# Kernel tuning notes

Hardware: AMD Instinct MI355X
Metric: run time of the kernel (lower is better)

The kernel has to match this reference:

```python
import jax, jax.numpy as jnp
import numpy as np

N_NODES = 50000
LEAKY_SLOPE = 0.2


def _degrees(idx, n):
    d = jax.ops.segment_sum(jnp.ones_like(idx, dtype=jnp.float32), idx, num_segments=n)
    return jnp.clip(d, 1.0)  # DGL clamps zero degrees to 1


def _gcn_layer(x, W, b, src, dst, out_inv_sqrt, in_inv_sqrt):
    # norm='both': h = D_in^{-1/2} A D_out^{-1/2} x, then x @ W + b
    h = x * out_inv_sqrt[:, None]
    agg = jax.ops.segment_sum(jnp.take(h, src, axis=0), dst, num_segments=N_NODES)
    agg = agg * in_inv_sqrt[:, None]
    return agg @ W + b


def setup_inputs() -> dict:
    key = jax.random.key(0)
    k1, k2, k3, k4, k5 = jax.random.split(key, 5)
    E = 800000
    init_emb = jax.random.normal(k1, (N_NODES, 300), dtype=jnp.float32)
    W1 = jax.random.normal(k2, (300, 400), dtype=jnp.float32) * (1.0 / np.sqrt(300.0))
    b1 = jnp.zeros((400,), dtype=jnp.float32)
    W2 = jax.random.normal(k3, (400, 512), dtype=jnp.float32) * (1.0 / np.sqrt(400.0))
    b2 = jnp.zeros((512,), dtype=jnp.float32)
    src = jax.random.randint(k4, (E,), 0, N_NODES, dtype=jnp.int32)
    dst = jax.random.randint(k5, (E,), 0, N_NODES, dtype=jnp.int32)
    return {"init_emb": init_emb, "W1": W1, "b1": b1, "W2": W2, "b2": b2,
            "src": src, "dst": dst}


def reference(init_emb, W1, b1, W2, b2, src, dst):
    out_inv_sqrt = jax.lax.rsqrt(_degrees(src, N_NODES))  # D_out^{-1/2}
    in_inv_sqrt = jax.lax.rsqrt(_degrees(dst, N_NODES))   # D_in^{-1/2}
    x = _gcn_layer(init_emb, W1, b1, src, dst, out_inv_sqrt, in_inv_sqrt)
    x = jnp.where(x >= 0, x, LEAKY_SLOPE * x)  # LeakyReLU(0.2); dropout = identity (eval)
    x = _gcn_layer(x, W2, b2, src, dst, out_inv_sqrt, in_inv_sqrt)
    return x
```

## Files before the change

### kernel.cpp

```cpp
#include <hip/hip_runtime.h>
#include <hip/hip_fp16.h>

#define NN   50000
#define NNP  50048
#define D0   300
#define K1   320
#define N1   400
#define K2   448
#define N2   512
#define NBLK 196

typedef __attribute__((ext_vector_type(8))) short bf16x8;
typedef __attribute__((ext_vector_type(4))) float f32x4;
typedef __attribute__((ext_vector_type(2))) float f32x2;
typedef __attribute__((ext_vector_type(4))) unsigned int u32x4;

__device__ __forceinline__ unsigned short f2bf(float x) {
    union { float f; unsigned u; } v; v.f = x;
    unsigned r = v.u + 0x7fffu + ((v.u >> 16) & 1u);
    return (unsigned short)(r >> 16);
}

__global__ __launch_bounds__(256) void pre_kernel(const int* __restrict__ src,
                                                  const int* __restrict__ dst,
                                                  int* __restrict__ cnt_s,
                                                  int* __restrict__ cnt_d, int E,
                                                  const float* __restrict__ W1,
                                                  const float* __restrict__ W2,
                                                  unsigned short* __restrict__ T1,
                                                  unsigned short* __restrict__ T2) {
    int tid = blockIdx.x * 256 + threadIdx.x;
    if (tid < E) {
        atomicAdd(&cnt_s[src[tid]], 1);
        atomicAdd(&cnt_d[dst[tid]], 1);
        return;
    }
    int u = tid - E;
    if (u < K2 * K1) {
        int n = u / K1, k = u - n * K1;
        float v = (n < N1 && k < D0) ? W1[k * N1 + n] : 0.f;
        T1[u] = f2bf(v);
    } else {
        u -= K2 * K1;
        if (u >= N2 * K2) return;
        int n = u / K2, k = u - n * K2;
        float v = (k < N1) ? W2[k * N2 + n] : 0.f;
        T2[u] = f2bf(v);
    }
}

__global__ __launch_bounds__(256) void scan_blk_kernel(const int* __restrict__ cnt,
                                                       int* __restrict__ offs,
                                                       int* __restrict__ bsum) {
    __shared__ int sh[256];
    int t = threadIdx.x, g = blockIdx.x * 256 + t;
    int v = (g < NN) ? cnt[g] : 0;
    sh[t] = v;
    __syncthreads();
    for (int off = 1; off < 256; off <<= 1) {
        int u = (t >= off) ? sh[t - off] : 0;
        __syncthreads();
        sh[t] += u;
        __syncthreads();
    }
    if (g < NN) offs[g] = sh[t] - v;
    if (t == 255) bsum[blockIdx.x] = sh[255];
}

__global__ __launch_bounds__(256) void scan_fix_kernel(int* __restrict__ offs,
                                                       const int* __restrict__ bsum,
                                                       const int* __restrict__ cnt_s,
                                                       const int* __restrict__ cnt_d,
                                                       float* __restrict__ deg_s,
                                                       float* __restrict__ deg_d, int E) {
    __shared__ int sh[256];
    int t = threadIdx.x;
    int v = (t < NBLK) ? bsum[t] : 0;
    sh[t] = v;
    __syncthreads();
    for (int off = 1; off < 256; off <<= 1) {
        int u = (t >= off) ? sh[t - off] : 0;
        __syncthreads();
        sh[t] += u;
        __syncthreads();
    }
    int myboff = (blockIdx.x > 0) ? sh[blockIdx.x - 1] : 0;
    int g = blockIdx.x * 256 + t;
    if (g < NN) {
        offs[g] += myboff;
        deg_s[g] = rsqrtf(fmaxf((float)cnt_s[g], 1.0f));
        deg_d[g] = rsqrtf(fmaxf((float)cnt_d[g], 1.0f));
    }
    if (g == NN) offs[NN] = E;
}

__global__ __launch_bounds__(256) void scat_emb_kernel(
    const int* __restrict__ src, const int* __restrict__ dst,
    const int* __restrict__ offs, int* __restrict__ cursor,
    int* __restrict__ ssrc, int E,
    const float* __restrict__ emb, const float* __restrict__ deg_s,
    __half* __restrict__ embh) {
    int tid = blockIdx.x * 256 + threadIdx.x;
    if (tid < E) {
        int d = dst[tid];
        int pos = atomicAdd(&cursor[d], 1);
        ssrc[offs[d] + pos] = src[tid];
        return;
    }
    int u = tid - E;
    const int CPR = K1 / 4;
    if (u >= NN * CPR) return;
    int node = u / CPR, c = u - node * CPR;
    int f = 4 * c;
    __half h[4] = {__half(0.f), __half(0.f), __half(0.f), __half(0.f)};
    if (f < D0) {
        float sc = deg_s[node];
        float4 v = *(const float4*)(emb + (size_t)node * D0 + f);
        h[0] = __float2half(v.x * sc); h[1] = __float2half(v.y * sc);
        h[2] = __float2half(v.z * sc); h[3] = __float2half(v.w * sc);
    }
    *(uint2*)(embh + (size_t)node * K1 + f) = *(uint2*)h;
}

template <int KP>
__global__ __launch_bounds__(256) void agg_h_kernel(
    const __half* __restrict__ X, const int* __restrict__ offs,
    const int* __restrict__ ssrc, const float* __restrict__ nscale,
    unsigned short* __restrict__ O) {
    constexpr int D8 = KP / 8;
    int node = blockIdx.x * 4 + (threadIdx.x >> 6);
    if (node >= NNP) return;
    int l = threadIdx.x & 63;
    bool act = l < D8;
    const uint4* Xq = (const uint4*)X;

    float a[8] = {0.f, 0.f, 0.f, 0.f, 0.f, 0.f, 0.f, 0.f};

#define ACCUM(U) { const __half2* hp = (const __half2*)&(U);                        \
                   float2 f0 = __half22float2(hp[0]), f1 = __half22float2(hp[1]);   \
                   float2 f2 = __half22float2(hp[2]), f3 = __half22float2(hp[3]);   \
                   a[0] += f0.x; a[1] += f0.y; a[2] += f1.x; a[3] += f1.y;          \
                   a[4] += f2.x; a[5] += f2.y; a[6] += f3.x; a[7] += f3.y; }

    if (node < NN) {
        int j = offs[node], end = offs[node + 1];
        for (; j + 8 <= end; j += 8) {
            uint4 u0, u1, u2, u3, u4, u5, u6, u7;
            int s0 = ssrc[j + 0], s1 = ssrc[j + 1], s2 = ssrc[j + 2], s3 = ssrc[j + 3];
            int s4 = ssrc[j + 4], s5 = ssrc[j + 5], s6 = ssrc[j + 6], s7 = ssrc[j + 7];
            if (act) {
                u0 = Xq[(size_t)s0 * D8 + l]; u1 = Xq[(size_t)s1 * D8 + l];
                u2 = Xq[(size_t)s2 * D8 + l]; u3 = Xq[(size_t)s3 * D8 + l];
                u4 = Xq[(size_t)s4 * D8 + l]; u5 = Xq[(size_t)s5 * D8 + l];
                u6 = Xq[(size_t)s6 * D8 + l]; u7 = Xq[(size_t)s7 * D8 + l];
                ACCUM(u0); ACCUM(u1); ACCUM(u2); ACCUM(u3);
                ACCUM(u4); ACCUM(u5); ACCUM(u6); ACCUM(u7);
            }
        }
        for (; j + 2 <= end; j += 2) {
            int s0 = ssrc[j + 0], s1 = ssrc[j + 1];
            if (act) {
                uint4 u0 = Xq[(size_t)s0 * D8 + l];
                uint4 u1 = Xq[(size_t)s1 * D8 + l];
                ACCUM(u0); ACCUM(u1);
            }
        }
        for (; j < end; ++j) {
            int s0 = ssrc[j];
            if (act) { uint4 u0 = Xq[(size_t)s0 * D8 + l]; ACCUM(u0); }
        }
        float ns = nscale[node];
#pragma unroll
        for (int i = 0; i < 8; ++i) a[i] *= ns;
    }
#undef ACCUM

    if (act) {
        unsigned short hv[8];
#pragma unroll
        for (int i = 0; i < 8; ++i) hv[i] = f2bf(a[i]);
        __builtin_nontemporal_store(*(u32x4*)hv, (u32x4*)(O + (size_t)node * KP + 8 * l));
    }
}

__global__ __launch_bounds__(256) void agg_q_kernel(
    const unsigned char* __restrict__ X, const int* __restrict__ offs,
    const int* __restrict__ ssrc, const float* __restrict__ nscale,
    unsigned short* __restrict__ O) {
    constexpr int D16 = 25;
    constexpr int OS  = 28;
    int w = threadIdx.x >> 6, l = threadIdx.x & 63;
    int half = l >> 5, sl = l & 31;
    int node = blockIdx.x * 8 + w * 2 + half;
    bool act = sl < D16;
    const uint4* Xq = (const uint4*)X;

    float a[16];
#pragma unroll
    for (int i = 0; i < 16; ++i) a[i] = 0.f;

#define ACCQ(U) { f32x2 p;                                                          \
    p = __builtin_amdgcn_cvt_pk_f32_fp8((int)(U).x, false); a[0]+=p.x;  a[1]+=p.y;  \
    p = __builtin_amdgcn_cvt_pk_f32_fp8((int)(U).x, true);  a[2]+=p.x;  a[3]+=p.y;  \
    p = __builtin_amdgcn_cvt_pk_f32_fp8((int)(U).y, false); a[4]+=p.x;  a[5]+=p.y;  \
    p = __builtin_amdgcn_cvt_pk_f32_fp8((int)(U).y, true);  a[6]+=p.x;  a[7]+=p.y;  \
    p = __builtin_amdgcn_cvt_pk_f32_fp8((int)(U).z, false); a[8]+=p.x;  a[9]+=p.y;  \
    p = __builtin_amdgcn_cvt_pk_f32_fp8((int)(U).z, true);  a[10]+=p.x; a[11]+=p.y; \
    p = __builtin_amdgcn_cvt_pk_f32_fp8((int)(U).w, false); a[12]+=p.x; a[13]+=p.y; \
    p = __builtin_amdgcn_cvt_pk_f32_fp8((int)(U).w, true);  a[14]+=p.x; a[15]+=p.y; }

    if (node < NN) {
        int j = offs[node], end = offs[node + 1];
        for (; j + 8 <= end; j += 8) {
            uint4 u0, u1, u2, u3, u4, u5, u6, u7;
            int s0 = ssrc[j + 0], s1 = ssrc[j + 1], s2 = ssrc[j + 2], s3 = ssrc[j + 3];
            int s4 = ssrc[j + 4], s5 = ssrc[j + 5], s6 = ssrc[j + 6], s7 = ssrc[j + 7];
            if (act) {
                u0 = Xq[(size_t)s0 * D16 + sl]; u1 = Xq[(size_t)s1 * D16 + sl];
                u2 = Xq[(size_t)s2 * D16 + sl]; u3 = Xq[(size_t)s3 * D16 + sl];
                u4 = Xq[(size_t)s4 * D16 + sl]; u5 = Xq[(size_t)s5 * D16 + sl];
                u6 = Xq[(size_t)s6 * D16 + sl]; u7 = Xq[(size_t)s7 * D16 + sl];
                ACCQ(u0); ACCQ(u1); ACCQ(u2); ACCQ(u3);
                ACCQ(u4); ACCQ(u5); ACCQ(u6); ACCQ(u7);
            }
        }
        for (; j + 2 <= end; j += 2) {
            int s0 = ssrc[j + 0], s1 = ssrc[j + 1];
            if (act) {
                uint4 u0 = Xq[(size_t)s0 * D16 + sl];
                uint4 u1 = Xq[(size_t)s1 * D16 + sl];
                ACCQ(u0); ACCQ(u1);
            }
        }
        for (; j < end; ++j) {
            int s0 = ssrc[j];
            if (act) { uint4 u0 = Xq[(size_t)s0 * D16 + sl]; ACCQ(u0); }
        }
        float ns = nscale[node];
#pragma unroll
        for (int i = 0; i < 16; ++i) a[i] *= ns;
    }
#undef ACCQ

    if (node < NNP && sl < OS) {
        unsigned short hv[16];
#pragma unroll
        for (int i = 0; i < 16; ++i) hv[i] = f2bf(a[i]);
        unsigned short* dst = O + (size_t)node * K2 + 16 * sl;
        __builtin_nontemporal_store(*(u32x4*)hv, (u32x4*)dst);
        __builtin_nontemporal_store(*(u32x4*)(hv + 8), (u32x4*)(dst + 8));
    }
}

template <int OMODE>
__global__ __launch_bounds__(256) void gemm_bf16_kernel(
    const unsigned short* __restrict__ A, const unsigned short* __restrict__ BT,
    const float* __restrict__ bias, const float* __restrict__ rs,
    void* __restrict__ Cv, int nbn, int Kpad, int Nvalid, int Cld) {
    constexpr int LDS_SHORTS = (OMODE == 0) ? 16384 : 12288;
    __shared__ __align__(16) unsigned short lds[LDS_SHORTS];
    const int AOF = 0, BOF = 8192;

    int nwg = (int)gridDim.x, orig = (int)blockIdx.x;
    int q8 = nwg >> 3, r8 = nwg & 7;
    int xc = orig & 7, o8 = orig >> 3;
    int wg = (xc < r8 ? xc * (q8 + 1) : r8 * (q8 + 1) + (xc - r8) * q8) + o8;
    int bn = wg % nbn, bm = wg / nbn;
    int m0 = bm * 128, n0 = bn * 64;

    int t = threadIdx.x, l = t & 63, w = t >> 6;
    int wm = w >> 1, wn = w & 1;

    f32x4 acc[4][2] = {};

    for (int k0 = 0; k0 < Kpad; k0 += 64) {
#pragma unroll
        for (int j = 0; j < 4; ++j) {
            int c = j * 256 + t;
            int r = c >> 3, qs = c & 7;
            size_t goff = (size_t)(m0 + r) * Kpad + k0 + ((qs ^ (r & 7)) << 3);
            int lbase = (j * 256 + w * 64) * 8;
            __builtin_amdgcn_global_load_lds(
                (const __attribute__((address_space(1))) void*)(A + goff),
                (__attribute__((address_space(3))) void*)&lds[AOF + lbase], 16, 0, 0);
        }
#pragma unroll
        for (int j = 0; j < 2; ++j) {
            int c = j * 256 + t;
            int r = c >> 3, qs = c & 7;
            size_t goff = (size_t)(n0 + r) * Kpad + k0 + ((qs ^ (r & 7)) << 3);
            int lbase = (j * 256 + w * 64) * 8;
            __builtin_amdgcn_global_load_lds(
                (const __attribute__((address_space(1))) void*)(BT + goff),
                (__attribute__((address_space(3))) void*)&lds[BOF + lbase], 16, 0, 0);
        }
        __syncthreads();

#pragma unroll
        for (int ks = 0; ks < 2; ++ks) {
            bf16x8 bfr[2];
#pragma unroll
            for (int ni = 0; ni < 2; ++ni) {
                int n = wn * 32 + ni * 16 + (l & 15);
                int slot = ks * 4 + (l >> 4);
                int idx = n * 64 + ((slot ^ (n & 7)) << 3);
                bfr[ni] = *(const bf16x8*)&lds[BOF + idx];
            }
#pragma unroll
            for (int mi = 0; mi < 4; ++mi) {
                int m = wm * 64 + mi * 16 + (l & 15);
                int slot = ks * 4 + (l >> 4);
                int idx = m * 64 + ((slot ^ (m & 7)) << 3);
                bf16x8 afr = *(const bf16x8*)&lds[AOF + idx];
#pragma unroll
                for (int ni = 0; ni < 2; ++ni)
                    acc[mi][ni] = __builtin_amdgcn_mfma_f32_16x16x32_bf16(afr, bfr[ni], acc[mi][ni], 0, 0, 0);
            }
        }
        __syncthreads();
    }

    if (OMODE == 0) {
        float* ltile = (float*)lds;
#pragma unroll
        for (int mi = 0; mi < 4; ++mi) {
            int rbase = wm * 64 + mi * 16 + ((l >> 4) << 2);
#pragma unroll
            for (int q = 0; q < 4; ++q) {
#pragma unroll
                for (int ni = 0; ni < 2; ++ni) {
                    int col = wn * 32 + ni * 16 + (l & 15);
                    ltile[(rbase + q) * 64 + col] = acc[mi][ni][q] + bias[n0 + col];
                }
            }
        }
        __syncthreads();
        const f32x4* lt4 = (const f32x4*)ltile;
#pragma unroll
        for (int it = 0; it < 8; ++it) {
            int idx = it * 256 + t;
            int r = idx >> 4, c4 = idx & 15;
            int m = m0 + r;
            if (m < NN) {
                f32x4 v = lt4[idx];
                __builtin_nontemporal_store(
                    v, (f32x4*)((float*)Cv + (size_t)m * Cld + n0 + c4 * 4));
            }
        }
    } else {
        unsigned char* ltile = (unsigned char*)lds;
#pragma unroll
        for (int mi = 0; mi < 4; ++mi) {
            int rbase = wm * 64 + mi * 16 + ((l >> 4) << 2);
#pragma unroll
            for (int q = 0; q < 4; ++q) {
                int m = m0 + rbase + q;
                float scale = (m < NN) ? rs[m] : 0.f;
#pragma unroll
                for (int ni = 0; ni < 2; ++ni) {
                    int col = wn * 32 + ni * 16 + (l & 15);
                    float v = acc[mi][ni][q] + bias[n0 + col];
                    v = v >= 0.f ? v : 0.2f * v;
                    v *= scale;
                    int pk = __builtin_amdgcn_cvt_pk_fp8_f32(v, v, 0, false);
                    ltile[(rbase + q) * 64 + col] = (unsigned char)(pk & 0xff);
                }
            }
        }
        __syncthreads();
        const u32x4* lt4 = (const u32x4*)ltile;
#pragma unroll
        for (int it = 0; it < 2; ++it) {
            int idx = it * 256 + t;
            int r = idx >> 2, ci = idx & 3;
            int m = m0 + r;
            int n = n0 + ci * 16;
            if (m < NN && n < Nvalid) {
                u32x4 v = lt4[idx];
                __builtin_nontemporal_store(
                    v, (u32x4*)((unsigned char*)Cv + (size_t)m * Cld + n));
            }
        }
    }
}

extern "C" void kernel_launch(void* const* d_in, const int* in_sizes, int n_in,
                              void* d_out, int out_size, void* d_ws, size_t ws_size,
                              hipStream_t stream) {
    const float* emb = (const float*)d_in[0];
    const float* W1  = (const float*)d_in[1];
    const float* b1  = (const float*)d_in[2];
    const float* W2  = (const float*)d_in[3];
    const float* b2  = (const float*)d_in[4];
    const int*   src = (const int*)d_in[5];
    const int*   dst = (const int*)d_in[6];
    const int E = in_sizes[5];

    unsigned short* A1   = (unsigned short*)d_ws;
    unsigned short* A2   = A1 + (size_t)NNP * K1;
    __half*         embh = (__half*)A2;
    unsigned short* W1T  = A2 + (size_t)NNP * K2;
    unsigned short* W2T  = W1T + (size_t)K2 * K1;

    unsigned char* h2  = (unsigned char*)d_out;
    float*         out = (float*)d_out;
    char* tail = (char*)d_out + (size_t)NN * N1;
    int* cnt_s  = (int*)tail;
    int* cnt_d  = cnt_s + NN;
    int* cursor = cnt_d + NN;
    int* offs   = cursor + NN;
    int* bsum   = offs + NN + 1;
    int* ssrc   = bsum + NBLK;
    float* deg_s = (float*)(ssrc + E);
    float* deg_d = deg_s + NN;

    hipMemsetAsync(cnt_s, 0, (size_t)(3 * NN) * sizeof(int), stream);

    {
        int total = E + K2 * K1 + N2 * K2;
        pre_kernel<<<(total + 255) / 256, 256, 0, stream>>>(
            src, dst, cnt_s, cnt_d, E, W1, W2, W1T, W2T);
    }
    scan_blk_kernel<<<NBLK, 256, 0, stream>>>(cnt_d, offs, bsum);
    scan_fix_kernel<<<NBLK, 256, 0, stream>>>(offs, bsum, cnt_s, cnt_d, deg_s, deg_d, E);

    {
        int total = E + NN * (K1 / 4);
        scat_emb_kernel<<<(total + 255) / 256, 256, 0, stream>>>(
            src, dst, offs, cursor, ssrc, E, emb, deg_s, embh);
    }

    agg_h_kernel<K1><<<NNP / 4, 256, 0, stream>>>(embh, offs, ssrc, deg_d, A1);

    gemm_bf16_kernel<1><<<391 * 7, 256, 0, stream>>>(
        A1, W1T, b1, deg_s, h2, 7, K1, N1, N1);

    agg_q_kernel<<<NNP / 8, 256, 0, stream>>>(h2, offs, ssrc, deg_d, A2);

    gemm_bf16_kernel<0><<<391 * 8, 256, 0, stream>>>(
        A2, W2T, b2, nullptr, out, 8, K2, N2, N2);
}
```

Before: 369.6 us.

## Partition edge scatter into destination-range slices for write locality

The CSR edge scatter is restructured so that each block handles a 4096-edge chunk and only the edges whose destination falls into one of 8 node-range slices. Each slice's atomics and ssrc writes then land in a narrower region of memory, improving cache and L2 locality. In exchange, every edge's dst is read 8 times and the scatter section launches more blocks with a loop instead of one thread per edge.

```diff
diff --git a/kernel.cpp b/kernel.cpp
--- a/kernel.cpp
+++ b/kernel.cpp
@@ -9,6 +9,8 @@
 #define K2   448
 #define N2   512
 #define NBLK 196
+#define EPB  4096
+#define NSL  8
 
 typedef __attribute__((ext_vector_type(8))) short bf16x8;
 typedef __attribute__((ext_vector_type(4))) float f32x4;
@@ -97,17 +99,26 @@
 __global__ __launch_bounds__(256) void scat_emb_kernel(
     const int* __restrict__ src, const int* __restrict__ dst,
     const int* __restrict__ offs, int* __restrict__ cursor,
-    int* __restrict__ ssrc, int E,
+    int* __restrict__ ssrc, int E, int nscat,
     const float* __restrict__ emb, const float* __restrict__ deg_s,
     __half* __restrict__ embh) {
-    int tid = blockIdx.x * 256 + threadIdx.x;
-    if (tid < E) {
-        int d = dst[tid];
-        int pos = atomicAdd(&cursor[d], 1);
-        ssrc[offs[d] + pos] = src[tid];
+    if ((int)blockIdx.x < nscat) {
+        int slice = blockIdx.x & (NSL - 1);
+        int chunk = blockIdx.x / NSL;
+        int lo = slice * (NN / NSL), hi = lo + (NN / NSL);
+        int base = chunk * EPB;
+        int lim = base + EPB; if (lim > E) lim = E;
+#pragma unroll 4
+        for (int i = base + (int)threadIdx.x; i < lim; i += 256) {
+            int d = dst[i];
+            if (d >= lo && d < hi) {
+                int pos = atomicAdd(&cursor[d], 1);
+                ssrc[offs[d] + pos] = src[i];
+            }
+        }
         return;
     }
-    int u = tid - E;
+    int u = ((int)blockIdx.x - nscat) * 256 + threadIdx.x;
     const int CPR = K1 / 4;
     if (u >= NN * CPR) return;
     int node = u / CPR, c = u - node * CPR;
@@ -425,9 +436,10 @@
     scan_fix_kernel<<<NBLK, 256, 0, stream>>>(offs, bsum, cnt_s, cnt_d, deg_s, deg_d, E);
 
     {
-        int total = E + NN * (K1 / 4);
-        scat_emb_kernel<<<(total + 255) / 256, 256, 0, stream>>>(
-            src, dst, offs, cursor, ssrc, E, emb, deg_s, embh);
+        int nscat = ((E + EPB - 1) / EPB) * NSL;
+        int nembh = (NN * (K1 / 4) + 255) / 256;
+        scat_emb_kernel<<<nscat + nembh, 256, 0, stream>>>(
+            src, dst, offs, cursor, ssrc, E, nscat, emb, deg_s, embh);
     }
 
     agg_h_kernel<K1><<<NNP / 4, 256, 0, stream>>>(embh, offs, ssrc, deg_d, A1);
```

Result: faster. 353.5 us (median of 2 runs) (-4.4%).
